# Kernel tuning notes

Hardware: AMD Instinct MI355X
Metric: run time of the kernel (lower is better)

Reference implementation:

```python
import jax, jax.numpy as jnp
import numpy as np

N = 25000
E = 400000
H = 4        # heads
C = 256      # per-head channels
D_IN = 1024
NEG_SLOPE = 0.2


def setup_inputs() -> dict:
    key = jax.random.key(0)
    k1, k2, k3, k4, k5, k6 = jax.random.split(key, 6)
    x = jax.random.normal(k1, (N, D_IN), dtype=jnp.float32)
    edge_index = jax.random.randint(k2, (2, E), 0, N, dtype=jnp.int64)
    # GATConv parameters
    scale = 1.0 / np.sqrt(D_IN)
    W = jax.random.normal(k3, (D_IN, H * C), dtype=jnp.float32) * scale
    att_src = jax.random.normal(k4, (H, C), dtype=jnp.float32) * 0.1
    att_dst = jax.random.normal(k5, (H, C), dtype=jnp.float32) * 0.1
    bias = jax.random.normal(k6, (H * C,), dtype=jnp.float32) * 0.01
    return {"x": x, "edge_index": edge_index, "W": W,
            "att_src": att_src, "att_dst": att_dst, "bias": bias}


def reference(x, edge_index, W, att_src, att_dst, bias):
    # Dense projection: [N, D_IN] @ [D_IN, H*C] -> [N, H, C]
    xp = (x @ W).reshape(N, H, C)

    # Per-node attention logits [N, H]
    a_src = jnp.einsum('nhc,hc->nh', xp, att_src)
    a_dst = jnp.einsum('nhc,hc->nh', xp, att_dst)

    # PyG default add_self_loops=True
    loops = jnp.arange(N, dtype=edge_index.dtype)
    src = jnp.concatenate([edge_index[0], loops])  # [E+N]
    dst = jnp.concatenate([edge_index[1], loops])  # [E+N]

    # Edge attention logits + LeakyReLU
    e = jax.nn.leaky_relu(a_src[src] + a_dst[dst], NEG_SLOPE)  # [E+N, H]

    # Segment softmax over destination nodes (every node has a self loop)
    m = jax.ops.segment_max(e, dst, num_segments=N)            # [N, H]
    ee = jnp.exp(e - m[dst])
    z = jax.ops.segment_sum(ee, dst, num_segments=N)           # [N, H]
    alpha = ee / z[dst]                                        # [E+N, H]

    # Scatter-weighted aggregation: out[i] = sum_j alpha_ij * xp[j]
    msgs = xp[src] * alpha[:, :, None]                         # [E+N, H, C]
    out = jax.ops.segment_sum(msgs, dst, num_segments=N)       # [N, H, C]

    out = out.reshape(N, H * C) + bias
    # dropout(0.5) is identity in eval mode; act = ReLU
    return jax.nn.relu(out)
```

## Files before the change

kernel.cpp:

```cpp
#include <hip/hip_runtime.h>
#include <hip/hip_bf16.h>
#include <stdint.h>

#define N_NODES 25000
#define M_PAD   25088
#define E_EDGES 400000
#define NE      (E_EDGES + N_NODES)
#define HEADS   4
#define D_DIM   1024
#define NEG_SLOPE 0.2f
#define NBLK_SCAN ((N_NODES + 255) / 256)

using bf16x8  = __attribute__((ext_vector_type(8))) short;
using floatx4 = __attribute__((ext_vector_type(4))) float;
using ushort8 = __attribute__((ext_vector_type(8))) unsigned short;

__device__ __forceinline__ unsigned short f2bf(float f) {
    union { float f; unsigned u; } v{f};
    unsigned r = v.u + 0x7fffu + ((v.u >> 16) & 1u);
    return (unsigned short)(r >> 16);
}
__device__ __forceinline__ float bf2f(unsigned short s) {
    union { unsigned u; float f; } v{(unsigned)s << 16};
    return v.f;
}

__global__ __launch_bounds__(256) void k_convert_x(
        const float* __restrict__ x, unsigned short* __restrict__ xb) {
    int i = blockIdx.x * 256 + threadIdx.x;
    int row = i >> 8;
    if (row >= M_PAD) return;
    ushort4 o;
    if (row < N_NODES) {
        float4 v = ((const float4*)x)[i];
        o = make_ushort4(f2bf(v.x), f2bf(v.y), f2bf(v.z), f2bf(v.w));
    } else {
        o = make_ushort4(0, 0, 0, 0);
    }
    ((ushort4*)xb)[i] = o;
}

__global__ void k_convert_wt(const float* __restrict__ W,
                             unsigned short* __restrict__ Wt) {
    __shared__ float tile[32][33];
    int bx = blockIdx.x, by = blockIdx.y;
    int tx = threadIdx.x, ty = threadIdx.y;
    #pragma unroll
    for (int i = 0; i < 32; i += 8) {
        int k = by * 32 + ty + i;
        int n = bx * 32 + tx;
        tile[ty + i][tx] = W[(size_t)k * D_DIM + n];
    }
    __syncthreads();
    #pragma unroll
    for (int i = 0; i < 32; i += 8) {
        int n = bx * 32 + ty + i;
        int k = by * 32 + tx;
        Wt[(size_t)n * D_DIM + k] = f2bf(tile[tx][ty + i]);
    }
}

__global__ __launch_bounds__(256) void k_gemm(
        const unsigned short* __restrict__ A,
        const unsigned short* __restrict__ Bt,
        unsigned short* __restrict__ C) {
    __shared__ __align__(16) unsigned short As[128 * 32];
    __shared__ __align__(16) unsigned short Bs[128 * 32];

    const int tid  = threadIdx.x;
    const int m0   = blockIdx.x * 128;
    const int n0   = blockIdx.y * 128;
    const int wave = tid >> 6, lane = tid & 63;
    const int wm   = (wave & 1) * 64, wn = (wave >> 1) * 64;
    const int lrow = lane & 15;
    const int quad = lane >> 4;

    const int srow = (lane >> 2);
    const int scol = (lane & 3) * 8;

    floatx4 acc[4][4] = {};

    for (int k0 = 0; k0 < D_DIM; k0 += 32) {
        #pragma unroll
        for (int j = 0; j < 2; ++j) {
            int rbase = wave * 32 + j * 16;
            const unsigned short* ga =
                &A[(size_t)(m0 + rbase + srow) * D_DIM + k0 + scol];
            const unsigned short* gb =
                &Bt[(size_t)(n0 + rbase + srow) * D_DIM + k0 + scol];
            __builtin_amdgcn_global_load_lds(
                (const __attribute__((address_space(1))) void*)ga,
                (__attribute__((address_space(3))) void*)&As[rbase * 32],
                16, 0, 0);
            __builtin_amdgcn_global_load_lds(
                (const __attribute__((address_space(1))) void*)gb,
                (__attribute__((address_space(3))) void*)&Bs[rbase * 32],
                16, 0, 0);
        }
        __syncthreads();

        bf16x8 af[4], bfr[4];
        #pragma unroll
        for (int mi = 0; mi < 4; ++mi)
            af[mi] = *(const bf16x8*)(&As[(wm + mi * 16 + lrow) * 32 + quad * 8]);
        #pragma unroll
        for (int ni = 0; ni < 4; ++ni)
            bfr[ni] = *(const bf16x8*)(&Bs[(wn + ni * 16 + lrow) * 32 + quad * 8]);

        #pragma unroll
        for (int mi = 0; mi < 4; ++mi)
            #pragma unroll
            for (int ni = 0; ni < 4; ++ni)
                acc[mi][ni] = __builtin_amdgcn_mfma_f32_16x16x32_bf16(
                    af[mi], bfr[ni], acc[mi][ni], 0, 0, 0);
        __syncthreads();
    }

    #pragma unroll
    for (int mi = 0; mi < 4; ++mi) {
        #pragma unroll
        for (int ni = 0; ni < 4; ++ni) {
            #pragma unroll
            for (int r = 0; r < 4; ++r) {
                int gm = m0 + wm + mi * 16 + quad * 4 + r;
                int gn = n0 + wn + ni * 16 + lrow;
                C[(size_t)gm * D_DIM + gn] = f2bf(acc[mi][ni][r]);
            }
        }
    }
}

__global__ __launch_bounds__(256) void k_node_logits(
        const unsigned short* __restrict__ xp,
        const float* __restrict__ att_src, const float* __restrict__ att_dst,
        float* __restrict__ a_src, float* __restrict__ a_dst) {
    int n = blockIdx.x;
    int tid = threadIdx.x;
    int h = tid >> 6, lane = tid & 63;
    int c = h * 256 + lane * 4;
    ushort4 v  = *(const ushort4*)(&xp[(size_t)n * D_DIM + c]);
    float4 as  = *(const float4*)(&att_src[c]);
    float4 ad  = *(const float4*)(&att_dst[c]);
    float x0 = bf2f(v.x), x1 = bf2f(v.y), x2 = bf2f(v.z), x3 = bf2f(v.w);
    float s = x0 * as.x + x1 * as.y + x2 * as.z + x3 * as.w;
    float d = x0 * ad.x + x1 * ad.y + x2 * ad.z + x3 * ad.w;
    #pragma unroll
    for (int off = 32; off > 0; off >>= 1) {
        s += __shfl_down(s, off);
        d += __shfl_down(d, off);
    }
    if (lane == 0) { a_src[n * 4 + h] = s; a_dst[n * 4 + h] = d; }
}

__global__ __launch_bounds__(256) void k_deg(
        const int* __restrict__ ei, int* __restrict__ deg) {
    int e = blockIdx.x * 256 + threadIdx.x;
    if (e >= NE) return;
    int d = (e < E_EDGES) ? ei[E_EDGES + e] : (e - E_EDGES);
    atomicAdd(&deg[d], 1);
}

__global__ __launch_bounds__(256) void k_scan1(
        const int* __restrict__ deg, int* __restrict__ rowstart,
        int* __restrict__ blocksum) {
    __shared__ int smem[256];
    int i = blockIdx.x * 256 + threadIdx.x;
    int v = (i < N_NODES) ? deg[i] : 0;
    smem[threadIdx.x] = v;
    __syncthreads();
    #pragma unroll
    for (int off = 1; off < 256; off <<= 1) {
        int t = (threadIdx.x >= off) ? smem[threadIdx.x - off] : 0;
        __syncthreads();
        smem[threadIdx.x] += t;
        __syncthreads();
    }
    if (i < N_NODES) rowstart[i] = smem[threadIdx.x] - v;
    if (threadIdx.x == 255) blocksum[blockIdx.x] = smem[255];
}

__global__ __launch_bounds__(128) void k_scan2(
        const int* __restrict__ blocksum, int* __restrict__ blockoff) {
    __shared__ int smem[128];
    int v = (threadIdx.x < NBLK_SCAN) ? blocksum[threadIdx.x] : 0;
    smem[threadIdx.x] = v;
    __syncthreads();
    #pragma unroll
    for (int off = 1; off < 128; off <<= 1) {
        int t = (threadIdx.x >= off) ? smem[threadIdx.x - off] : 0;
        __syncthreads();
        smem[threadIdx.x] += t;
        __syncthreads();
    }
    blockoff[threadIdx.x] = smem[threadIdx.x] - v;
}

__global__ __launch_bounds__(256) void k_scan3(
        int* __restrict__ rowstart, const int* __restrict__ blockoff) {
    int i = blockIdx.x * 256 + threadIdx.x;
    if (i < N_NODES) rowstart[i] += blockoff[blockIdx.x];
    if (i == 0) rowstart[N_NODES] = NE;
}

__global__ __launch_bounds__(256) void k_edge_exp_scatter(
        const int* __restrict__ ei,
        const float* __restrict__ a_src, const float* __restrict__ a_dst,
        const int* __restrict__ rowstart, int* __restrict__ cursor,
        int* __restrict__ csr_src, float* __restrict__ csr_ee) {
    int e = blockIdx.x * 256 + threadIdx.x;
    if (e >= NE) return;
    int s, d;
    if (e < E_EDGES) { s = ei[e]; d = ei[E_EDGES + e]; }
    else             { s = d = e - E_EDGES; }
    float4 as = *(const float4*)(&a_src[s * 4]);
    float4 ad = *(const float4*)(&a_dst[d * 4]);
    float l0 = as.x + ad.x, l1 = as.y + ad.y, l2 = as.z + ad.z, l3 = as.w + ad.w;
    l0 = l0 > 0.f ? l0 : NEG_SLOPE * l0;
    l1 = l1 > 0.f ? l1 : NEG_SLOPE * l1;
    l2 = l2 > 0.f ? l2 : NEG_SLOPE * l2;
    l3 = l3 > 0.f ? l3 : NEG_SLOPE * l3;
    int pos  = atomicAdd(&cursor[d], 1);
    int slot = rowstart[d] + pos;
    csr_src[slot] = s;
    *(float4*)(&csr_ee[(size_t)slot * 4]) =
        make_float4(__expf(l0), __expf(l1), __expf(l2), __expf(l3));
}

__device__ __forceinline__ void acc8(float* acc, float a, ushort8 v) {
    #pragma unroll
    for (int j = 0; j < 8; ++j) acc[j] += a * bf2f((unsigned short)v[j]);
}

__global__ __launch_bounds__(256) void k_node_aggregate(
        const int* __restrict__ csr_src, const float* __restrict__ csr_ee,
        const int* __restrict__ rowstart,
        const unsigned short* __restrict__ xp,
        const float* __restrict__ bias, float* __restrict__ out) {
    const int tid  = threadIdx.x;
    const int half = tid >> 7;
    const int n    = blockIdx.x * 2 + half;
    const int t    = tid & 127;
    const int row  = rowstart[n];
    const int deg  = rowstart[n + 1] - row;

    __shared__ float zsh[2][4];
    if ((tid & 64) == 0) {
        int lane = tid & 63;
        float z0 = 0.f, z1 = 0.f, z2 = 0.f, z3 = 0.f;
        for (int i = lane; i < deg; i += 64) {
            float4 v = *(const float4*)(&csr_ee[(size_t)(row + i) * 4]);
            z0 += v.x; z1 += v.y; z2 += v.z; z3 += v.w;
        }
        #pragma unroll
        for (int off = 32; off > 0; off >>= 1) {
            z0 += __shfl_down(z0, off);
            z1 += __shfl_down(z1, off);
            z2 += __shfl_down(z2, off);
            z3 += __shfl_down(z3, off);
        }
        if (lane == 0) {
            zsh[half][0] = z0; zsh[half][1] = z1;
            zsh[half][2] = z2; zsh[half][3] = z3;
        }
    }
    __syncthreads();

    const int h = t >> 5;
    const int c = t * 8;
    const float rz = 1.0f / zsh[half][h];

    float acc[8] = {};
    int i = 0;
    for (; i + 4 <= deg; i += 4) {
        int s0 = csr_src[row + i + 0];
        int s1 = csr_src[row + i + 1];
        int s2 = csr_src[row + i + 2];
        int s3 = csr_src[row + i + 3];
        float a0 = csr_ee[(size_t)(row + i + 0) * 4 + h] * rz;
        float a1 = csr_ee[(size_t)(row + i + 1) * 4 + h] * rz;
        float a2 = csr_ee[(size_t)(row + i + 2) * 4 + h] * rz;
        float a3 = csr_ee[(size_t)(row + i + 3) * 4 + h] * rz;
        ushort8 v0 = *(const ushort8*)(&xp[(size_t)s0 * D_DIM + c]);
        ushort8 v1 = *(const ushort8*)(&xp[(size_t)s1 * D_DIM + c]);
        ushort8 v2 = *(const ushort8*)(&xp[(size_t)s2 * D_DIM + c]);
        ushort8 v3 = *(const ushort8*)(&xp[(size_t)s3 * D_DIM + c]);
        acc8(acc, a0, v0);
        acc8(acc, a1, v1);
        acc8(acc, a2, v2);
        acc8(acc, a3, v3);
    }
    for (; i < deg; ++i) {
        int s   = csr_src[row + i];
        float a = csr_ee[(size_t)(row + i) * 4 + h] * rz;
        ushort8 v = *(const ushort8*)(&xp[(size_t)s * D_DIM + c]);
        acc8(acc, a, v);
    }

    float4 b0 = *(const float4*)(&bias[c]);
    float4 b1 = *(const float4*)(&bias[c + 4]);
    float4 o0, o1;
    o0.x = fmaxf(acc[0] + b0.x, 0.f);
    o0.y = fmaxf(acc[1] + b0.y, 0.f);
    o0.z = fmaxf(acc[2] + b0.z, 0.f);
    o0.w = fmaxf(acc[3] + b0.w, 0.f);
    o1.x = fmaxf(acc[4] + b1.x, 0.f);
    o1.y = fmaxf(acc[5] + b1.y, 0.f);
    o1.z = fmaxf(acc[6] + b1.z, 0.f);
    o1.w = fmaxf(acc[7] + b1.w, 0.f);
    *(float4*)(&out[(size_t)n * D_DIM + c])     = o0;
    *(float4*)(&out[(size_t)n * D_DIM + c + 4]) = o1;
}

extern "C" void kernel_launch(void* const* d_in, const int* in_sizes, int n_in,
                              void* d_out, int out_size, void* d_ws, size_t ws_size,
                              hipStream_t stream) {
    const float* x       = (const float*)d_in[0];
    const int*   ei      = (const int*)d_in[1];
    const float* W       = (const float*)d_in[2];
    const float* att_src = (const float*)d_in[3];
    const float* att_dst = (const float*)d_in[4];
    const float* bias    = (const float*)d_in[5];
    float* out = (float*)d_out;

    char* ws = (char*)d_ws;
    size_t off = 0;
    auto alloc = [&](size_t bytes) -> void* {
        void* p = ws + off;
        off = (off + bytes + 255) & ~(size_t)255;
        return p;
    };
    unsigned short* xb   = (unsigned short*)alloc((size_t)M_PAD * D_DIM * 2);
    unsigned short* Wt   = (unsigned short*)alloc((size_t)D_DIM * D_DIM * 2);
    unsigned short* xpb  = (unsigned short*)alloc((size_t)M_PAD * D_DIM * 2);
    float* a_src    = (float*)alloc((size_t)N_NODES * 4 * 4);
    float* a_dst    = (float*)alloc((size_t)N_NODES * 4 * 4);
    int*   deg      = (int*)alloc((size_t)N_NODES * 4);
    int*   rowstart = (int*)alloc((size_t)(N_NODES + 1) * 4);
    int*   cursor   = (int*)alloc((size_t)N_NODES * 4);
    int*   blocksum = (int*)alloc((size_t)NBLK_SCAN * 4);
    int*   blockoff = (int*)alloc((size_t)128 * 4);
    int*   csr_src  = (int*)alloc((size_t)NE * 4);
    float* csr_ee   = (float*)alloc((size_t)NE * 4 * 4);

    hipMemsetAsync(deg, 0, (size_t)N_NODES * 4, stream);
    hipMemsetAsync(cursor, 0, (size_t)N_NODES * 4, stream);

    k_convert_x<<<M_PAD, 256, 0, stream>>>(x, xb);
    k_convert_wt<<<dim3(32, 32), dim3(32, 8), 0, stream>>>(W, Wt);
    k_gemm<<<dim3(M_PAD / 128, D_DIM / 128), 256, 0, stream>>>(xb, Wt, xpb);
    k_node_logits<<<N_NODES, 256, 0, stream>>>(xpb, att_src, att_dst, a_src, a_dst);
    k_deg<<<(NE + 255) / 256, 256, 0, stream>>>(ei, deg);
    k_scan1<<<NBLK_SCAN, 256, 0, stream>>>(deg, rowstart, blocksum);
    k_scan2<<<1, 128, 0, stream>>>(blocksum, blockoff);
    k_scan3<<<NBLK_SCAN, 256, 0, stream>>>(rowstart, blockoff);
    k_edge_exp_scatter<<<(NE + 255) / 256, 256, 0, stream>>>(
        ei, a_src, a_dst, rowstart, cursor, csr_src, csr_ee);
    k_node_aggregate<<<12500, 256, 0, stream>>>(
        csr_src, csr_ee, rowstart, xpb, bias, out);
}
```

Before: 457.9 us.

## Replace GEMM with 256x256 double-buffered swizzled-LDS MFMA kernel; deepen aggregation unroll

Rewrites the projection GEMM to use 256x256 tiles, 512 threads, a 64-wide K step, XOR-swizzled LDS layout and double-buffered asynchronous global-to-LDS staging that overlaps with MFMA, plus block-index remapping for L2 locality. The aim is higher arithmetic intensity and hidden load latency compared with the old 128x128 single-buffered loop. The aggregation kernel gains an 8-edge unrolled gather loop and applies the softmax normalisation once at the end instead of per edge. The GEMM adds more register and LDS pressure (128KB LDS) and hand-tuned waitcnt logic that is fragile.

```diff
diff --git a/kernel.cpp b/kernel.cpp
--- a/kernel.cpp
+++ b/kernel.cpp
@@ -60,74 +60,143 @@
     }
 }
 
-__global__ __launch_bounds__(256) void k_gemm(
+__device__ __forceinline__ void stage_half16(
+        const unsigned short* __restrict__ g,
+        unsigned short* lds_half,
+        int wave, int rl, int sl8) {
+    #pragma unroll
+    for (int j = 0; j < 2; ++j) {
+        const int R = j * 64 + wave * 8;
+        __builtin_amdgcn_global_load_lds(
+            (const __attribute__((address_space(1))) void*)
+                (g + (size_t)(R + rl) * 1024 + sl8),
+            (__attribute__((address_space(3))) void*)(lds_half + R * 64),
+            16, 0, 0);
+    }
+}
+
+__global__ __launch_bounds__(512, 2) void k_gemm256(
         const unsigned short* __restrict__ A,
         const unsigned short* __restrict__ Bt,
         unsigned short* __restrict__ C) {
-    __shared__ __align__(16) unsigned short As[128 * 32];
-    __shared__ __align__(16) unsigned short Bs[128 * 32];
+    __shared__ unsigned short lds[65536];
 
     const int tid  = threadIdx.x;
-    const int m0   = blockIdx.x * 128;
-    const int n0   = blockIdx.y * 128;
     const int wave = tid >> 6, lane = tid & 63;
-    const int wm   = (wave & 1) * 64, wn = (wave >> 1) * 64;
-    const int lrow = lane & 15;
-    const int quad = lane >> 4;
-
-    const int srow = (lane >> 2);
-    const int scol = (lane & 3) * 8;
-
-    floatx4 acc[4][4] = {};
-
-    for (int k0 = 0; k0 < D_DIM; k0 += 32) {
-        #pragma unroll
-        for (int j = 0; j < 2; ++j) {
-            int rbase = wave * 32 + j * 16;
-            const unsigned short* ga =
-                &A[(size_t)(m0 + rbase + srow) * D_DIM + k0 + scol];
-            const unsigned short* gb =
-                &Bt[(size_t)(n0 + rbase + srow) * D_DIM + k0 + scol];
-            __builtin_amdgcn_global_load_lds(
-                (const __attribute__((address_space(1))) void*)ga,
-                (__attribute__((address_space(3))) void*)&As[rbase * 32],
-                16, 0, 0);
-            __builtin_amdgcn_global_load_lds(
-                (const __attribute__((address_space(1))) void*)gb,
-                (__attribute__((address_space(3))) void*)&Bs[rbase * 32],
-                16, 0, 0);
+    const int lrow = lane & 15, quad = lane >> 4;
+    const int wm   = wave >> 2, wn = wave & 3;
+    const int rl   = lane >> 3;
+    const int sl8  = ((lane & 7) ^ rl) * 8;
+
+    const int wg = (blockIdx.x & 7) * 49 + (blockIdx.x >> 3);
+    const int m0 = (wg % 98) * 256;
+    const int n0 = (wg / 98) * 256;
+
+    const unsigned short* Am = A  + (size_t)m0 * 1024;
+    const unsigned short* Bn = Bt + (size_t)n0 * 1024;
+
+    const int colk0 = (quad * 8)      ^ ((lrow & 7) << 3);
+    const int colk1 = (32 + quad * 8) ^ ((lrow & 7) << 3);
+
+    floatx4 acc[8][4] = {};
+
+    stage_half16(Bn,                          lds + 16384,               wave, rl, sl8);
+    stage_half16(Bn + (size_t)128 * 1024,     lds + 16384 + 8192,        wave, rl, sl8);
+    stage_half16(Am,                          lds,                       wave, rl, sl8);
+    stage_half16(Am + (size_t)128 * 1024,     lds + 8192,                wave, rl, sl8);
+    stage_half16(Bn + 64,                     lds + 49152,               wave, rl, sl8);
+    stage_half16(Bn + (size_t)128 * 1024 + 64, lds + 49152 + 8192,       wave, rl, sl8);
+    stage_half16(Am + 64,                     lds + 32768,               wave, rl, sl8);
+    asm volatile("s_waitcnt vmcnt(6)" ::: "memory");
+    __builtin_amdgcn_sched_barrier(0);
+    __builtin_amdgcn_s_barrier();
+
+    #pragma unroll 1
+    for (int it = 0; it < 8; ++it) {
+        const int t   = it * 2;
+        const int kt1 = t * 64 + 64, kt2 = t * 64 + 128, kt3 = t * 64 + 192;
+        const bool s1 = kt2 < 1024;
+        const bool s2 = kt3 < 1024;
+        #pragma unroll
+        for (int hb = 0; hb < 2; ++hb) {
+            const unsigned short* LAc = lds + hb * 32768;
+            const unsigned short* LBc = LAc + 16384;
+            bf16x8 bfr[4][2];
+            #pragma unroll
+            for (int q = 0; q < 4; ++q) {
+                bf16x8 af[2][2];
+                #pragma unroll
+                for (int j = 0; j < 2; ++j) {
+                    const int ar = (wm * 128 + (2 * q + j) * 16 + lrow) * 64;
+                    af[j][0] = *(const bf16x8*)(LAc + ar + colk0);
+                    af[j][1] = *(const bf16x8*)(LAc + ar + colk1);
+                }
+                if (q == 0) {
+                    #pragma unroll
+                    for (int ni = 0; ni < 4; ++ni) {
+                        const int br = (wn * 64 + ni * 16 + lrow) * 64;
+                        bfr[ni][0] = *(const bf16x8*)(LBc + br + colk0);
+                        bfr[ni][1] = *(const bf16x8*)(LBc + br + colk1);
+                    }
+                }
+                if (hb == 0) {
+                    if (q == 0)
+                        stage_half16(Am + (size_t)128 * 1024 + kt1,
+                                     lds + 32768 + 8192, wave, rl, sl8);
+                    if (q == 1 && s1)
+                        stage_half16(Bn + kt2, lds + 16384, wave, rl, sl8);
+                    if (q == 2 && s1)
+                        stage_half16(Bn + (size_t)128 * 1024 + kt2,
+                                     lds + 16384 + 8192, wave, rl, sl8);
+                    if (q == 3 && s1)
+                        stage_half16(Am + kt2, lds, wave, rl, sl8);
+                } else {
+                    if (q == 0 && s1)
+                        stage_half16(Am + (size_t)128 * 1024 + kt2,
+                                     lds + 8192, wave, rl, sl8);
+                    if (q == 1 && s2)
+                        stage_half16(Bn + kt3, lds + 49152, wave, rl, sl8);
+                    if (q == 2 && s2)
+                        stage_half16(Bn + (size_t)128 * 1024 + kt3,
+                                     lds + 49152 + 8192, wave, rl, sl8);
+                    if (q == 3 && s2)
+                        stage_half16(Am + kt3, lds + 32768, wave, rl, sl8);
+                }
+                if (q == 3) {
+                    const bool full = (hb == 0) ? s1 : s2;
+                    if (full) asm volatile("s_waitcnt vmcnt(6)" ::: "memory");
+                    else      asm volatile("s_waitcnt vmcnt(0)" ::: "memory");
+                    __builtin_amdgcn_sched_barrier(0);
+                }
+                __builtin_amdgcn_s_barrier();
+                asm volatile("s_waitcnt lgkmcnt(0)" ::: "memory");
+                __builtin_amdgcn_sched_barrier(0);
+                __builtin_amdgcn_s_setprio(1);
+                #pragma unroll
+                for (int j = 0; j < 2; ++j)
+                    #pragma unroll
+                    for (int ni = 0; ni < 4; ++ni) {
+                        acc[2*q+j][ni] = __builtin_amdgcn_mfma_f32_16x16x32_bf16(
+                            af[j][0], bfr[ni][0], acc[2*q+j][ni], 0, 0, 0);
+                        acc[2*q+j][ni] = __builtin_amdgcn_mfma_f32_16x16x32_bf16(
+                            af[j][1], bfr[ni][1], acc[2*q+j][ni], 0, 0, 0);
+                    }
+                __builtin_amdgcn_s_setprio(0);
+                __builtin_amdgcn_s_barrier();
+            }
         }
-        __syncthreads();
-
-        bf16x8 af[4], bfr[4];
-        #pragma unroll
-        for (int mi = 0; mi < 4; ++mi)
-            af[mi] = *(const bf16x8*)(&As[(wm + mi * 16 + lrow) * 32 + quad * 8]);
+    }
+
+    #pragma unroll
+    for (int mi = 0; mi < 8; ++mi)
         #pragma unroll
         for (int ni = 0; ni < 4; ++ni)
-            bfr[ni] = *(const bf16x8*)(&Bs[(wn + ni * 16 + lrow) * 32 + quad * 8]);
-
-        #pragma unroll
-        for (int mi = 0; mi < 4; ++mi)
-            #pragma unroll
-            for (int ni = 0; ni < 4; ++ni)
-                acc[mi][ni] = __builtin_amdgcn_mfma_f32_16x16x32_bf16(
-                    af[mi], bfr[ni], acc[mi][ni], 0, 0, 0);
-        __syncthreads();
-    }
-
-    #pragma unroll
-    for (int mi = 0; mi < 4; ++mi) {
-        #pragma unroll
-        for (int ni = 0; ni < 4; ++ni) {
             #pragma unroll
             for (int r = 0; r < 4; ++r) {
-                int gm = m0 + wm + mi * 16 + quad * 4 + r;
-                int gn = n0 + wn + ni * 16 + lrow;
-                C[(size_t)gm * D_DIM + gn] = f2bf(acc[mi][ni][r]);
+                int gm = m0 + wm * 128 + mi * 16 + quad * 4 + r;
+                int gn = n0 + wn * 64 + ni * 16 + lrow;
+                C[(size_t)gm * 1024 + gn] = f2bf(acc[mi][ni][r]);
             }
-        }
-    }
 }
 
 __global__ __launch_bounds__(256) void k_node_logits(
@@ -271,15 +340,29 @@
 
     float acc[8] = {};
     int i = 0;
+    for (; i + 8 <= deg; i += 8) {
+        int s[8];
+        float a[8];
+        #pragma unroll
+        for (int u = 0; u < 8; ++u) s[u] = csr_src[row + i + u];
+        #pragma unroll
+        for (int u = 0; u < 8; ++u) a[u] = csr_ee[(size_t)(row + i + u) * 4 + h];
+        ushort8 v[8];
+        #pragma unroll
+        for (int u = 0; u < 8; ++u)
+            v[u] = *(const ushort8*)(&xp[(size_t)s[u] * D_DIM + c]);
+        #pragma unroll
+        for (int u = 0; u < 8; ++u) acc8(acc, a[u], v[u]);
+    }
     for (; i + 4 <= deg; i += 4) {
         int s0 = csr_src[row + i + 0];
         int s1 = csr_src[row + i + 1];
         int s2 = csr_src[row + i + 2];
         int s3 = csr_src[row + i + 3];
-        float a0 = csr_ee[(size_t)(row + i + 0) * 4 + h] * rz;
-        float a1 = csr_ee[(size_t)(row + i + 1) * 4 + h] * rz;
-        float a2 = csr_ee[(size_t)(row + i + 2) * 4 + h] * rz;
-        float a3 = csr_ee[(size_t)(row + i + 3) * 4 + h] * rz;
+        float a0 = csr_ee[(size_t)(row + i + 0) * 4 + h];
+        float a1 = csr_ee[(size_t)(row + i + 1) * 4 + h];
+        float a2 = csr_ee[(size_t)(row + i + 2) * 4 + h];
+        float a3 = csr_ee[(size_t)(row + i + 3) * 4 + h];
         ushort8 v0 = *(const ushort8*)(&xp[(size_t)s0 * D_DIM + c]);
         ushort8 v1 = *(const ushort8*)(&xp[(size_t)s1 * D_DIM + c]);
         ushort8 v2 = *(const ushort8*)(&xp[(size_t)s2 * D_DIM + c]);
@@ -291,10 +374,12 @@
     }
     for (; i < deg; ++i) {
         int s   = csr_src[row + i];
-        float a = csr_ee[(size_t)(row + i) * 4 + h] * rz;
+        float a = csr_ee[(size_t)(row + i) * 4 + h];
         ushort8 v = *(const ushort8*)(&xp[(size_t)s * D_DIM + c]);
         acc8(acc, a, v);
     }
+    #pragma unroll
+    for (int j = 0; j < 8; ++j) acc[j] *= rz;
 
     float4 b0 = *(const float4*)(&bias[c]);
     float4 b1 = *(const float4*)(&bias[c + 4]);
@@ -347,7 +432,7 @@
 
     k_convert_x<<<M_PAD, 256, 0, stream>>>(x, xb);
     k_convert_wt<<<dim3(32, 32), dim3(32, 8), 0, stream>>>(W, Wt);
-    k_gemm<<<dim3(M_PAD / 128, D_DIM / 128), 256, 0, stream>>>(xb, Wt, xpb);
+    k_gemm256<<<dim3(M_PAD / 256 * (D_DIM / 256)), 512, 0, stream>>>(xb, Wt, xpb);
     k_node_logits<<<N_NODES, 256, 0, stream>>>(xpb, att_src, att_dst, a_src, a_dst);
     k_deg<<<(NE + 255) / 256, 256, 0, stream>>>(ei, deg);
     k_scan1<<<NBLK_SCAN, 256, 0, stream>>>(deg, rowstart, blocksum);
```

After: 444.5 us. 1.03x faster.
